# Optimization experiments

Measured on AMD Instinct MI355X. Metric: run time of the kernel, lower is better.

Reference implementation:

```python
import jax, jax.numpy as jnp
import numpy as np

B, T, S, I, H = 64, 64, 512, 512, 512

def setup_inputs() -> dict:
    key = jax.random.key(0)
    ks = jax.random.split(key, 9)
    sc = 0.02
    return {
        "input": jax.random.normal(ks[0], (B, T, I), jnp.float32),
        "h0": jax.random.normal(ks[1], (B, H), jnp.float32),
        "c0": jax.random.normal(ks[2], (B, H), jnp.float32),
        "ctx": jax.random.normal(ks[3], (S, B, H), jnp.float32),
        "W_ih": jax.random.normal(ks[4], (4 * H, I), jnp.float32) * sc,
        "b_ih": jax.random.normal(ks[5], (4 * H,), jnp.float32) * sc,
        "W_hh": jax.random.normal(ks[6], (4 * H, H), jnp.float32) * sc,
        "b_hh": jax.random.normal(ks[7], (4 * H,), jnp.float32) * sc,
        "W_out": jax.random.normal(ks[8], (H, 2 * H), jnp.float32) * sc,
    }

def reference(input, h0, c0, ctx, W_ih, b_ih, W_hh, b_hh, W_out):
    ctx_b = ctx.transpose(1, 0, 2)          # (B, S, H)
    x_tm = input.transpose(1, 0, 2)          # (T, B, I) time-major

    def step(carry, x):
        hx, cx = carry
        gates = x @ W_ih.T + b_ih + hx @ W_hh.T + b_hh   # (B, 4H)
        i, f, g, o = jnp.split(gates, 4, axis=1)          # chunk order: in, forget, cell, out
        ct = jax.nn.sigmoid(f) * cx + jax.nn.sigmoid(i) * jnp.tanh(g)
        ht = jax.nn.sigmoid(o) * jnp.tanh(ct)
        # dot attention over source positions
        scores = jnp.einsum('bsh,bh->bs', ctx_b, ht)      # (B, S)
        attn = jax.nn.softmax(scores, axis=1)
        wc = jnp.einsum('bs,bsh->bh', attn, ctx_b)        # (B, H)
        h_tilde = jnp.tanh(jnp.concatenate([wc, ht], axis=1) @ W_out.T)
        return (ht, ct), h_tilde

    (hT, cT), out = jax.lax.scan(step, (h0, c0), x_tm)    # out: (T, B, H)
    return out.transpose(1, 0, 2), hT, cT
```

## Files before the change

### kernel.cpp

```cpp
#include <hip/hip_runtime.h>
#include <hip/hip_bf16.h>

#define NB 64
#define NT_ 64
#define NS 512
#define NI 512
#define NH 512
#define G4 2048
#define H2 1024
#define BT (NB*NT_)
#define RBLK 64
#define CPB 8

typedef __attribute__((ext_vector_type(8))) short short8;
typedef __attribute__((ext_vector_type(4))) float f32x4;

__device__ __forceinline__ short f2bs(float f) {
    __hip_bfloat16 h = __float2bfloat16(f);
    return *reinterpret_cast<short*>(&h);
}
__device__ __forceinline__ float bs2f(short s) {
    unsigned int u = ((unsigned int)(unsigned short)s) << 16;
    union { unsigned int u; float f; } c; c.u = u; return c.f;
}
__device__ __forceinline__ short8 ld8b(const __hip_bfloat16* p) {
    return *reinterpret_cast<const short8*>(p);
}
__device__ __forceinline__ void ld8f2(const float* p, short8& hi, short8& lo) {
    float4 a = *reinterpret_cast<const float4*>(p);
    float4 b = *reinterpret_cast<const float4*>(p + 4);
    float v[8] = {a.x,a.y,a.z,a.w,b.x,b.y,b.z,b.w};
    #pragma unroll
    for (int i = 0; i < 8; i++) {
        short h = f2bs(v[i]);
        hi[i] = h;
        lo[i] = f2bs(v[i] - bs2f(h));
    }
}
__device__ __forceinline__ float fsigm(float x){ return 1.f/(1.f + __expf(-x)); }
__device__ __forceinline__ float ftanh(float x){ float e = __expf(2.f*x); return 1.f - 2.f/(e + 1.f); }

__global__ __launch_bounds__(256) void conv_split(const float* __restrict__ s,
                                                  __hip_bfloat16* __restrict__ hi,
                                                  __hip_bfloat16* __restrict__ lo, int n) {
    for (int i = blockIdx.x*256 + threadIdx.x; i < n; i += gridDim.x*256) {
        float x = s[i];
        __hip_bfloat16 h = __float2bfloat16(x);
        hi[i] = h;
        lo[i] = __float2bfloat16(x - __bfloat162float(h));
    }
}

__global__ __launch_bounds__(256) void hseq0_init(const float* __restrict__ h0,
                                                  __hip_bfloat16* __restrict__ hs_h,
                                                  __hip_bfloat16* __restrict__ hs_l,
                                                  unsigned* __restrict__ flags) {
    int i = blockIdx.x*256 + threadIdx.x;
    if (i < RBLK*32) flags[i] = 0u;
    if (i < NB*NH) {
        float x = h0[i];
        __hip_bfloat16 h = __float2bfloat16(x);
        hs_h[i] = h;
        hs_l[i] = __float2bfloat16(x - __bfloat162float(h));
    }
}

__global__ __launch_bounds__(256) void transpose_ctx(const float* __restrict__ ctx,
                                                     __hip_bfloat16* __restrict__ ctxT) {
    __shared__ float tile[64][65];
    int s0 = blockIdx.x*64, h0 = blockIdx.y*64, b = blockIdx.z;
    int tx = threadIdx.x & 63, ty = threadIdx.x >> 6;
    for (int i = 0; i < 16; i++) {
        int s = i*4 + ty;
        tile[s][tx] = ctx[(size_t)(s0+s)*NB*NH + (size_t)b*NH + h0 + tx];
    }
    __syncthreads();
    for (int i = 0; i < 16; i++) {
        int h = i*4 + ty;
        ctxT[(size_t)b*NH*NS + (size_t)(h0+h)*NS + s0 + tx] = __float2bfloat16(tile[tx][h]);
    }
}

__global__ __launch_bounds__(256) void gemm_xw(const __hip_bfloat16* __restrict__ Xh,
                                               const __hip_bfloat16* __restrict__ Xl,
                                               const __hip_bfloat16* __restrict__ Wh,
                                               const __hip_bfloat16* __restrict__ Wl,
                                               const float* __restrict__ b_ih,
                                               const float* __restrict__ b_hh,
                                               float* __restrict__ XW) {
    int wid = blockIdx.x*4 + (threadIdx.x>>6);
    int lane = threadIdx.x & 63;
    int m0 = (wid >> 5) * 64;
    int n0 = (wid & 31) * 64;
    int fr = lane & 15, fq = lane >> 4;
    f32x4 acc[4][4] = {};
    for (int kk = 0; kk < NI; kk += 32) {
        short8 ah[4], al[4], bh[4], bl[4];
        #pragma unroll
        for (int i = 0; i < 4; i++) {
            size_t off = (size_t)(m0+i*16+fr)*NI + kk + fq*8;
            ah[i] = ld8b(Xh + off);
            al[i] = ld8b(Xl + off);
        }
        #pragma unroll
        for (int j = 0; j < 4; j++) {
            bh[j] = ld8b(Wh + (size_t)(n0+j*16+fr)*NI + kk + fq*8);
            bl[j] = ld8b(Wl + (size_t)(n0+j*16+fr)*NI + kk + fq*8);
        }
        #pragma unroll
        for (int i = 0; i < 4; i++)
            #pragma unroll
            for (int j = 0; j < 4; j++) {
                acc[i][j] = __builtin_amdgcn_mfma_f32_16x16x32_bf16(ah[i], bh[j], acc[i][j], 0,0,0);
                acc[i][j] = __builtin_amdgcn_mfma_f32_16x16x32_bf16(ah[i], bl[j], acc[i][j], 0,0,0);
                acc[i][j] = __builtin_amdgcn_mfma_f32_16x16x32_bf16(al[i], bh[j], acc[i][j], 0,0,0);
            }
    }
    #pragma unroll
    for (int i = 0; i < 4; i++)
      #pragma unroll
      for (int j = 0; j < 4; j++)
        #pragma unroll
        for (int r = 0; r < 4; r++) {
            int m = m0 + i*16 + fq*4 + r;
            int n = n0 + j*16 + fr;
            XW[(size_t)m*G4 + n] = acc[i][j][r] + b_ih[n] + b_hh[n];
        }
}

__global__ __launch_bounds__(256, 1) void lstm_persist(
    const float* __restrict__ c0,
    const __hip_bfloat16* __restrict__ Whh_h,
    const __hip_bfloat16* __restrict__ Whh_l,
    const float* __restrict__ XW,
    __hip_bfloat16* __restrict__ hs_h,
    __hip_bfloat16* __restrict__ hs_l,
    float* __restrict__ hT, float* __restrict__ cT,
    unsigned* __restrict__ flags)
{
    __shared__ __hip_bfloat16 Wh[32*512];
    __shared__ __hip_bfloat16 Wl[32*512];
    __shared__ float gl[4][32][33];
    int tid = threadIdx.x, bi = blockIdx.x;
    int lane = tid & 63, w = tid >> 6;
    int fr = lane & 15, fq = lane >> 4;

    {
        int jl = tid >> 3, ck8 = tid & 7;
        int grow = (jl >> 3) * NH + bi * CPB + (jl & 7);
        const short8* srcH = (const short8*)(Whh_h + (size_t)grow * NH);
        const short8* srcL = (const short8*)(Whh_l + (size_t)grow * NH);
        #pragma unroll
        for (int cc = 0; cc < 8; cc++) {
            int ck = ck8 * 8 + cc;
            int sw = (ck * 16) ^ ((jl & 7) << 4);
            *(short8*)((char*)Wh + jl * 1024 + sw) = srcH[ck];
            *(short8*)((char*)Wl + jl * 1024 + sw) = srcL[ck];
        }
    }
    int eb  = tid >> 2;
    int ec0 = (tid & 3) * 2;
    int ebl = eb & 31, mhalf = eb >> 5;
    float creg[2];
    creg[0] = c0[eb * NH + bi*CPB + ec0];
    creg[1] = c0[eb * NH + bi*CPB + ec0 + 1];
    float xw[8];
    #pragma unroll
    for (int g = 0; g < 4; g++)
      #pragma unroll
      for (int u = 0; u < 2; u++)
        xw[g*2+u] = XW[(size_t)eb*NT_*G4 + g*NH + bi*CPB + ec0 + u];
    __syncthreads();

    int m0 = (w & 1) * 32;
    int kbase = (w >> 1) * 256;

    for (int t = 0; t < NT_; t++) {
        const __hip_bfloat16* Ah = hs_h + (size_t)t * NB * NH;
        const __hip_bfloat16* Al = hs_l + (size_t)t * NB * NH;

        short8 Aregh[2][8], Aregl[2][8];
        #pragma unroll
        for (int i = 0; i < 2; i++) {
            const __hip_bfloat16* rowH = Ah + (size_t)(m0 + i*16 + fr) * NH + kbase + fq*8;
            const __hip_bfloat16* rowL = Al + (size_t)(m0 + i*16 + fr) * NH + kbase + fq*8;
            #pragma unroll
            for (int k8 = 0; k8 < 8; k8++) {
                Aregh[i][k8] = ld8b(rowH + k8*32);
                Aregl[i][k8] = ld8b(rowL + k8*32);
            }
        }

        f32x4 acc[2][2] = {};
        #pragma unroll
        for (int k8 = 0; k8 < 8; k8++) {
            short8 b_h[2], b_l[2];
            #pragma unroll
            for (int j = 0; j < 2; j++) {
                int jl = j*16 + fr;
                int byt = jl*1024 + ((((kbase + k8*32 + fq*8)*2)) ^ ((jl & 7) << 4));
                b_h[j] = *(const short8*)((const char*)Wh + byt);
                b_l[j] = *(const short8*)((const char*)Wl + byt);
            }
            #pragma unroll
            for (int i = 0; i < 2; i++)
                #pragma unroll
                for (int j = 0; j < 2; j++) {
                    acc[i][j] = __builtin_amdgcn_mfma_f32_16x16x32_bf16(Aregh[i][k8], b_h[j], acc[i][j], 0,0,0);
                    acc[i][j] = __builtin_amdgcn_mfma_f32_16x16x32_bf16(Aregh[i][k8], b_l[j], acc[i][j], 0,0,0);
                    acc[i][j] = __builtin_amdgcn_mfma_f32_16x16x32_bf16(Aregl[i][k8], b_h[j], acc[i][j], 0,0,0);
                }
        }
        #pragma unroll
        for (int i = 0; i < 2; i++)
          #pragma unroll
          for (int j = 0; j < 2; j++)
            #pragma unroll
            for (int r = 0; r < 4; r++)
                gl[w][i*16 + fq*4 + r][j*16 + fr] = acc[i][j][r];
        __syncthreads();

        float hv[2];
        #pragma unroll
        for (int u = 0; u < 2; u++) {
            int cl = ec0 + u;
            float gi = gl[mhalf][ebl][cl]      + gl[2+mhalf][ebl][cl]      + xw[u];
            float gf = gl[mhalf][ebl][8 + cl]  + gl[2+mhalf][ebl][8 + cl]  + xw[2+u];
            float gg = gl[mhalf][ebl][16 + cl] + gl[2+mhalf][ebl][16 + cl] + xw[4+u];
            float go = gl[mhalf][ebl][24 + cl] + gl[2+mhalf][ebl][24 + cl] + xw[6+u];
            float ct = fsigm(gf)*creg[u] + fsigm(gi)*ftanh(gg);
            hv[u] = fsigm(go)*ftanh(ct);
            creg[u] = ct;
        }
        int hcol = bi*CPB + ec0;
        size_t hoff = (size_t)(t+1)*NB*NH + (size_t)eb*NH + hcol;
        unsigned short h0b = (unsigned short)f2bs(hv[0]);
        unsigned short h1b = (unsigned short)f2bs(hv[1]);
        unsigned ph = (unsigned)h0b | ((unsigned)h1b << 16);
        unsigned short l0b = (unsigned short)f2bs(hv[0] - bs2f((short)h0b));
        unsigned short l1b = (unsigned short)f2bs(hv[1] - bs2f((short)h1b));
        unsigned pl = (unsigned)l0b | ((unsigned)l1b << 16);
        __hip_atomic_store((unsigned*)&hs_h[hoff], ph, __ATOMIC_RELAXED, __HIP_MEMORY_SCOPE_AGENT);
        __hip_atomic_store((unsigned*)&hs_l[hoff], pl, __ATOMIC_RELAXED, __HIP_MEMORY_SCOPE_AGENT);
        if (t == NT_-1) {
            *(float2*)&hT[(size_t)eb*NH + hcol] = make_float2(hv[0], hv[1]);
            *(float2*)&cT[(size_t)eb*NH + hcol] = make_float2(creg[0], creg[1]);
        }

        asm volatile("s_waitcnt vmcnt(0)" ::: "memory");
        __syncthreads();
        if (tid == 0)
            __hip_atomic_store(&flags[bi*32], (unsigned)(t+1), __ATOMIC_RELAXED, __HIP_MEMORY_SCOPE_AGENT);
        if (t + 1 < NT_) {
            #pragma unroll
            for (int g = 0; g < 4; g++)
              #pragma unroll
              for (int u = 0; u < 2; u++)
                xw[g*2+u] = XW[((size_t)eb*NT_ + (t+1))*G4 + g*NH + bi*CPB + ec0 + u];
        }
        {
            unsigned target = (unsigned)(t+1);
            int guard = 0;
            while (__hip_atomic_load(&flags[lane*32], __ATOMIC_RELAXED, __HIP_MEMORY_SCOPE_AGENT) < target) {
                __builtin_amdgcn_s_sleep(1);
                if (++guard > (1<<22)) break;
            }
        }
    }
}

__global__ __launch_bounds__(256) void gemm_scores(const __hip_bfloat16* __restrict__ hs_h,
                                                   const __hip_bfloat16* __restrict__ hs_l,
                                                   const float* __restrict__ ctx,
                                                   float* __restrict__ scores) {
    int wid = blockIdx.x*4 + (threadIdx.x>>6);
    int lane = threadIdx.x & 63;
    int b  = wid >> 3;
    int n0 = (wid & 7) * 64;
    int fr = lane & 15, fq = lane >> 4;
    const __hip_bfloat16* Abh = hs_h + NB*NH + (size_t)b*NH;
    const __hip_bfloat16* Abl = hs_l + NB*NH + (size_t)b*NH;
    const float* Bb = ctx + (size_t)b*NH;
    f32x4 acc[4][4] = {};
    for (int kk = 0; kk < NH; kk += 32) {
        short8 ah[4], al[4], bh[4], bl[4];
        #pragma unroll
        for (int i = 0; i < 4; i++) {
            size_t off = (size_t)(i*16+fr)*NB*NH + kk + fq*8;
            ah[i] = ld8b(Abh + off);
            al[i] = ld8b(Abl + off);
        }
        #pragma unroll
        for (int j = 0; j < 4; j++) ld8f2(Bb + (size_t)(n0+j*16+fr)*NB*NH + kk + fq*8, bh[j], bl[j]);
        #pragma unroll
        for (int i = 0; i < 4; i++)
            #pragma unroll
            for (int j = 0; j < 4; j++) {
                acc[i][j] = __builtin_amdgcn_mfma_f32_16x16x32_bf16(ah[i], bh[j], acc[i][j], 0,0,0);
                acc[i][j] = __builtin_amdgcn_mfma_f32_16x16x32_bf16(ah[i], bl[j], acc[i][j], 0,0,0);
                acc[i][j] = __builtin_amdgcn_mfma_f32_16x16x32_bf16(al[i], bh[j], acc[i][j], 0,0,0);
            }
    }
    #pragma unroll
    for (int i = 0; i < 4; i++)
      #pragma unroll
      for (int j = 0; j < 4; j++)
        #pragma unroll
        for (int r = 0; r < 4; r++) {
            int t = i*16 + fq*4 + r;
            int s = n0 + j*16 + fr;
            scores[((size_t)b*NT_ + t)*NS + s] = acc[i][j][r];
        }
}

__global__ __launch_bounds__(256) void softmax_rows(const float* __restrict__ scores,
                                                    __hip_bfloat16* __restrict__ ah,
                                                    __hip_bfloat16* __restrict__ al) {
    int row = blockIdx.x*4 + (threadIdx.x>>6);
    int lane = threadIdx.x & 63;
    const float* r = scores + (size_t)row*NS;
    float v[8], mx = -1e30f;
    #pragma unroll
    for (int i = 0; i < 8; i++) { v[i] = r[lane + i*64]; mx = fmaxf(mx, v[i]); }
    #pragma unroll
    for (int off = 32; off; off >>= 1) mx = fmaxf(mx, __shfl_xor(mx, off));
    float sum = 0.f;
    #pragma unroll
    for (int i = 0; i < 8; i++) { v[i] = __expf(v[i]-mx); sum += v[i]; }
    #pragma unroll
    for (int off = 32; off; off >>= 1) sum += __shfl_xor(sum, off);
    float inv = 1.f/sum;
    #pragma unroll
    for (int i = 0; i < 8; i++) {
        float a = v[i]*inv;
        __hip_bfloat16 h = __float2bfloat16(a);
        ah[(size_t)row*NS + lane + i*64] = h;
        al[(size_t)row*NS + lane + i*64] = __float2bfloat16(a - __bfloat162float(h));
    }
}

__global__ __launch_bounds__(256) void gemm_wc(const __hip_bfloat16* __restrict__ Ah,
                                               const __hip_bfloat16* __restrict__ Al,
                                               const __hip_bfloat16* __restrict__ ctxT,
                                               float* __restrict__ Wc) {
    int wid = blockIdx.x*4 + (threadIdx.x>>6);
    int lane = threadIdx.x & 63;
    int b  = wid >> 3;
    int n0 = (wid & 7) * 64;
    int fr = lane & 15, fq = lane >> 4;
    const __hip_bfloat16* Abh = Ah + (size_t)b*NT_*NS;
    const __hip_bfloat16* Abl = Al + (size_t)b*NT_*NS;
    const __hip_bfloat16* Bb  = ctxT + (size_t)b*NH*NS;
    f32x4 acc[4][4] = {};
    for (int kk = 0; kk < NS; kk += 32) {
        short8 ah[4], al[4], bb[4];
        #pragma unroll
        for (int i = 0; i < 4; i++) {
            ah[i] = ld8b(Abh + (size_t)(i*16+fr)*NS + kk + fq*8);
            al[i] = ld8b(Abl + (size_t)(i*16+fr)*NS + kk + fq*8);
        }
        #pragma unroll
        for (int j = 0; j < 4; j++) bb[j] = ld8b(Bb + (size_t)(n0+j*16+fr)*NS + kk + fq*8);
        #pragma unroll
        for (int i = 0; i < 4; i++)
            #pragma unroll
            for (int j = 0; j < 4; j++) {
                acc[i][j] = __builtin_amdgcn_mfma_f32_16x16x32_bf16(ah[i], bb[j], acc[i][j], 0,0,0);
                acc[i][j] = __builtin_amdgcn_mfma_f32_16x16x32_bf16(al[i], bb[j], acc[i][j], 0,0,0);
            }
    }
    #pragma unroll
    for (int i = 0; i < 4; i++)
      #pragma unroll
      for (int j = 0; j < 4; j++)
        #pragma unroll
        for (int r = 0; r < 4; r++) {
            int t = i*16 + fq*4 + r;
            int h = n0 + j*16 + fr;
            Wc[((size_t)b*NT_ + t)*NH + h] = acc[i][j][r];
        }
}

__global__ __launch_bounds__(256) void gemm_out(const float* __restrict__ Wc,
                                                const __hip_bfloat16* __restrict__ hs_h,
                                                const __hip_bfloat16* __restrict__ hs_l,
                                                const __hip_bfloat16* __restrict__ Wh,
                                                const __hip_bfloat16* __restrict__ Wl,
                                                float* __restrict__ out) {
    int wid = blockIdx.x*4 + (threadIdx.x>>6);
    int lane = threadIdx.x & 63;
    int m0 = (wid >> 3) * 64;
    int n0 = (wid & 7) * 64;
    int fr = lane & 15, fq = lane >> 4;
    f32x4 acc[4][4] = {};
    for (int kk = 0; kk < NH; kk += 32) {
        short8 ah[4], al[4], bh[4], bl[4];
        #pragma unroll
        for (int i = 0; i < 4; i++) ld8f2(Wc + (size_t)(m0+i*16+fr)*NH + kk + fq*8, ah[i], al[i]);
        #pragma unroll
        for (int j = 0; j < 4; j++) {
            bh[j] = ld8b(Wh + (size_t)(n0+j*16+fr)*H2 + kk + fq*8);
            bl[j] = ld8b(Wl + (size_t)(n0+j*16+fr)*H2 + kk + fq*8);
        }
        #pragma unroll
        for (int i = 0; i < 4; i++)
            #pragma unroll
            for (int j = 0; j < 4; j++) {
                acc[i][j] = __builtin_amdgcn_mfma_f32_16x16x32_bf16(ah[i], bh[j], acc[i][j], 0,0,0);
                acc[i][j] = __builtin_amdgcn_mfma_f32_16x16x32_bf16(ah[i], bl[j], acc[i][j], 0,0,0);
                acc[i][j] = __builtin_amdgcn_mfma_f32_16x16x32_bf16(al[i], bh[j], acc[i][j], 0,0,0);
            }
    }
    {
        const __hip_bfloat16* A2h = hs_h + NB*NH + (size_t)(m0>>6)*NH;
        const __hip_bfloat16* A2l = hs_l + NB*NH + (size_t)(m0>>6)*NH;
        for (int kk = 0; kk < NH; kk += 32) {
            short8 ah[4], al[4], bh[4], bl[4];
            #pragma unroll
            for (int i = 0; i < 4; i++) {
                size_t off = (size_t)(i*16+fr)*NB*NH + kk + fq*8;
                ah[i] = ld8b(A2h + off);
                al[i] = ld8b(A2l + off);
            }
            #pragma unroll
            for (int j = 0; j < 4; j++) {
                bh[j] = ld8b(Wh + (size_t)(n0+j*16+fr)*H2 + NH + kk + fq*8);
                bl[j] = ld8b(Wl + (size_t)(n0+j*16+fr)*H2 + NH + kk + fq*8);
            }
            #pragma unroll
            for (int i = 0; i < 4; i++)
                #pragma unroll
                for (int j = 0; j < 4; j++) {
                    acc[i][j] = __builtin_amdgcn_mfma_f32_16x16x32_bf16(ah[i], bh[j], acc[i][j], 0,0,0);
                    acc[i][j] = __builtin_amdgcn_mfma_f32_16x16x32_bf16(ah[i], bl[j], acc[i][j], 0,0,0);
                    acc[i][j] = __builtin_amdgcn_mfma_f32_16x16x32_bf16(al[i], bh[j], acc[i][j], 0,0,0);
                }
        }
    }
    #pragma unroll
    for (int i = 0; i < 4; i++)
      #pragma unroll
      for (int j = 0; j < 4; j++)
        #pragma unroll
        for (int r = 0; r < 4; r++) {
            int m = m0 + i*16 + fq*4 + r;
            int n = n0 + j*16 + fr;
            out[(size_t)m*NH + n] = ftanh(acc[i][j][r]);
        }
}


extern "C" void kernel_launch(void* const* d_in, const int* in_sizes, int n_in,
                              void* d_out, int out_size, void* d_ws, size_t ws_size,
                              hipStream_t stream) {
    const float* input = (const float*)d_in[0];
    const float* h0    = (const float*)d_in[1];
    const float* c0    = (const float*)d_in[2];
    const float* ctx   = (const float*)d_in[3];
    const float* W_ih  = (const float*)d_in[4];
    const float* b_ih  = (const float*)d_in[5];
    const float* W_hh  = (const float*)d_in[6];
    const float* b_hh  = (const float*)d_in[7];
    const float* W_out = (const float*)d_in[8];
    float* out = (float*)d_out;

    const size_t OFF_XW     = 0;
    const size_t OFF_SCORES = 0;
    const size_t OFF_ATTN_H = 8388608;
    const size_t OFF_ATTN_L = 12582912;
    const size_t OFF_HS_H   = 33554432;
    const size_t OFF_HS_L   = 37814272;
    const size_t OFF_FLAGS  = 42074112;
    const size_t OFF_WC     = 42082304;
    const size_t OFF_XH     = 42082304;
    const size_t OFF_XL     = 46276608;
    const size_t OFF_WIH_H  = 50470912;
    const size_t OFF_WIH_L  = 52568064;
    const size_t OFF_WHH_H  = 54665216;
    const size_t OFF_WHH_L  = 56762368;
    const size_t OFF_WOUT_H = 58859520;
    const size_t OFF_WOUT_L = 59908096;
    const size_t OFF_CTXT   = 60956672;
    if (ws_size < 94511104u) return;

    char* ws = (char*)d_ws;
    float*          XW     = (float*)(ws + OFF_XW);
    float*          scores = (float*)(ws + OFF_SCORES);
    __hip_bfloat16* attn_h = (__hip_bfloat16*)(ws + OFF_ATTN_H);
    __hip_bfloat16* attn_l = (__hip_bfloat16*)(ws + OFF_ATTN_L);
    __hip_bfloat16* hs_h   = (__hip_bfloat16*)(ws + OFF_HS_H);
    __hip_bfloat16* hs_l   = (__hip_bfloat16*)(ws + OFF_HS_L);
    unsigned*       flags  = (unsigned*)(ws + OFF_FLAGS);
    float*          Wc     = (float*)(ws + OFF_WC);
    __hip_bfloat16* Xh     = (__hip_bfloat16*)(ws + OFF_XH);
    __hip_bfloat16* Xl     = (__hip_bfloat16*)(ws + OFF_XL);
    __hip_bfloat16* Wih_h  = (__hip_bfloat16*)(ws + OFF_WIH_H);
    __hip_bfloat16* Wih_l  = (__hip_bfloat16*)(ws + OFF_WIH_L);
    __hip_bfloat16* Whh_h  = (__hip_bfloat16*)(ws + OFF_WHH_H);
    __hip_bfloat16* Whh_l  = (__hip_bfloat16*)(ws + OFF_WHH_L);
    __hip_bfloat16* Wout_h = (__hip_bfloat16*)(ws + OFF_WOUT_H);
    __hip_bfloat16* Wout_l = (__hip_bfloat16*)(ws + OFF_WOUT_L);
    __hip_bfloat16* ctxT   = (__hip_bfloat16*)(ws + OFF_CTXT);

    conv_split<<<2048, 256, 0, stream>>>(W_ih, Wih_h, Wih_l, G4*NI);
    conv_split<<<2048, 256, 0, stream>>>(W_hh, Whh_h, Whh_l, G4*NH);
    conv_split<<<1024, 256, 0, stream>>>(W_out, Wout_h, Wout_l, NH*H2);
    conv_split<<<2048, 256, 0, stream>>>(input, Xh, Xl, BT*NI);
    hseq0_init<<<128, 256, 0, stream>>>(h0, hs_h, hs_l, flags);
    gemm_xw<<<512, 256, 0, stream>>>(Xh, Xl, Wih_h, Wih_l, b_ih, b_hh, XW);

    float* hT = out + (size_t)BT*NH;
    float* cT = hT + NB*NH;
    lstm_persist<<<RBLK, 256, 0, stream>>>(c0, Whh_h, Whh_l, XW, hs_h, hs_l, hT, cT, flags);

    transpose_ctx<<<dim3(8,8,64), 256, 0, stream>>>(ctx, ctxT);
    gemm_scores<<<128, 256, 0, stream>>>(hs_h, hs_l, ctx, scores);
    softmax_rows<<<1024, 256, 0, stream>>>(scores, attn_h, attn_l);
    gemm_wc<<<128, 256, 0, stream>>>(attn_h, attn_l, ctxT, Wc);
    gemm_out<<<128, 256, 0, stream>>>(Wc, hs_h, hs_l, Wout_h, Wout_l, out);
}
```

Before: 666.9 us.

## Replace flag-based grid barrier with sentinel-polled data-driven sync in persistent LSTM

Drops the per-step global flag barrier in the persistent LSTM kernel. Consumers now poll the hidden-state buffers directly, which are pre-filled with 0xFFFFFFFF sentinels, until valid data appears. The gate scratch is double-buffered so only one block barrier per step remains, and the XOR swizzle of the weight tile is replaced with row padding. The aim is to remove the full grid-wide flag round-trip and its extra barriers per timestep. The cost is filling a large sentinel region in the init kernel, and correctness now depends on bf16 pairs never legitimately equalling the sentinel pattern.

```diff
diff --git a/kernel.cpp b/kernel.cpp
--- a/kernel.cpp
+++ b/kernel.cpp
@@ -11,6 +11,7 @@
 #define BT (NB*NT_)
 #define RBLK 64
 #define CPB 8
+#define WROW 528
 
 typedef __attribute__((ext_vector_type(8))) short short8;
 typedef __attribute__((ext_vector_type(4))) float f32x4;
@@ -25,6 +26,14 @@
 }
 __device__ __forceinline__ short8 ld8b(const __hip_bfloat16* p) {
     return *reinterpret_cast<const short8*>(p);
+}
+__device__ __forceinline__ short8 mk8(unsigned long long a, unsigned long long b) {
+    union { unsigned long long q[2]; short8 s; } u;
+    u.q[0] = a; u.q[1] = b;
+    return u.s;
+}
+__device__ __forceinline__ bool okq(unsigned long long q) {
+    return ((unsigned)q != 0xFFFFFFFFu) && ((unsigned)(q >> 32) != 0xFFFFFFFFu);
 }
 __device__ __forceinline__ void ld8f2(const float* p, short8& hi, short8& lo) {
     float4 a = *reinterpret_cast<const float4*>(p);
@@ -53,15 +62,25 @@
 
 __global__ __launch_bounds__(256) void hseq0_init(const float* __restrict__ h0,
                                                   __hip_bfloat16* __restrict__ hs_h,
-                                                  __hip_bfloat16* __restrict__ hs_l,
-                                                  unsigned* __restrict__ flags) {
+                                                  __hip_bfloat16* __restrict__ hs_l) {
     int i = blockIdx.x*256 + threadIdx.x;
-    if (i < RBLK*32) flags[i] = 0u;
-    if (i < NB*NH) {
-        float x = h0[i];
-        __hip_bfloat16 h = __float2bfloat16(x);
-        hs_h[i] = h;
-        hs_l[i] = __float2bfloat16(x - __bfloat162float(h));
+    const int nsent = NB*NH*NT_/2;
+    unsigned* ph = (unsigned*)(hs_h + NB*NH);
+    unsigned* pl = (unsigned*)(hs_l + NB*NH);
+    for (int k = i; k < nsent; k += gridDim.x*256) {
+        __hip_atomic_store(&ph[k], 0xFFFFFFFFu, __ATOMIC_RELAXED, __HIP_MEMORY_SCOPE_AGENT);
+        __hip_atomic_store(&pl[k], 0xFFFFFFFFu, __ATOMIC_RELAXED, __HIP_MEMORY_SCOPE_AGENT);
+    }
+    if (i < NB*NH/2) {
+        float v0 = h0[2*i], v1 = h0[2*i+1];
+        unsigned short h0b = (unsigned short)f2bs(v0);
+        unsigned short h1b = (unsigned short)f2bs(v1);
+        unsigned short l0b = (unsigned short)f2bs(v0 - bs2f((short)h0b));
+        unsigned short l1b = (unsigned short)f2bs(v1 - bs2f((short)h1b));
+        __hip_atomic_store((unsigned*)hs_h + i, (unsigned)h0b | ((unsigned)h1b << 16),
+                           __ATOMIC_RELAXED, __HIP_MEMORY_SCOPE_AGENT);
+        __hip_atomic_store((unsigned*)hs_l + i, (unsigned)l0b | ((unsigned)l1b << 16),
+                           __ATOMIC_RELAXED, __HIP_MEMORY_SCOPE_AGENT);
     }
 }
 
@@ -135,12 +154,11 @@
     const float* __restrict__ XW,
     __hip_bfloat16* __restrict__ hs_h,
     __hip_bfloat16* __restrict__ hs_l,
-    float* __restrict__ hT, float* __restrict__ cT,
-    unsigned* __restrict__ flags)
+    float* __restrict__ hT, float* __restrict__ cT)
 {
-    __shared__ __hip_bfloat16 Wh[32*512];
-    __shared__ __hip_bfloat16 Wl[32*512];
-    __shared__ float gl[4][32][33];
+    __shared__ __hip_bfloat16 Wh[32*WROW];
+    __shared__ __hip_bfloat16 Wl[32*WROW];
+    __shared__ float gl[2][4][32][33];
     int tid = threadIdx.x, bi = blockIdx.x;
     int lane = tid & 63, w = tid >> 6;
     int fr = lane & 15, fq = lane >> 4;
@@ -153,9 +171,8 @@
         #pragma unroll
         for (int cc = 0; cc < 8; cc++) {
             int ck = ck8 * 8 + cc;
-            int sw = (ck * 16) ^ ((jl & 7) << 4);
-            *(short8*)((char*)Wh + jl * 1024 + sw) = srcH[ck];
-            *(short8*)((char*)Wl + jl * 1024 + sw) = srcL[ck];
+            *(short8*)((char*)Wh + jl*(WROW*2) + ck*16) = srcH[ck];
+            *(short8*)((char*)Wl + jl*(WROW*2) + ck*16) = srcL[ck];
         }
     }
     int eb  = tid >> 2;
@@ -176,19 +193,39 @@
     int kbase = (w >> 1) * 256;
 
     for (int t = 0; t < NT_; t++) {
-        const __hip_bfloat16* Ah = hs_h + (size_t)t * NB * NH;
-        const __hip_bfloat16* Al = hs_l + (size_t)t * NB * NH;
-
-        short8 Aregh[2][8], Aregl[2][8];
-        #pragma unroll
-        for (int i = 0; i < 2; i++) {
-            const __hip_bfloat16* rowH = Ah + (size_t)(m0 + i*16 + fr) * NH + kbase + fq*8;
-            const __hip_bfloat16* rowL = Al + (size_t)(m0 + i*16 + fr) * NH + kbase + fq*8;
-            #pragma unroll
-            for (int k8 = 0; k8 < 8; k8++) {
-                Aregh[i][k8] = ld8b(rowH + k8*32);
-                Aregl[i][k8] = ld8b(rowL + k8*32);
-            }
+        int p = t & 1;
+
+        unsigned long long qa[2][8][2], ql[2][8][2];
+        {
+            const char* bH0 = (const char*)(hs_h + (size_t)t*NB*NH + (size_t)(m0+fr)*NH + kbase);
+            const char* bL0 = (const char*)(hs_l + (size_t)t*NB*NH + (size_t)(m0+fr)*NH + kbase);
+            const char* bH1 = bH0 + 16*NH*2;
+            const char* bL1 = bL0 + 16*NH*2;
+            int guard = 0; bool ok;
+            do {
+                ok = true;
+                #pragma unroll
+                for (int i = 0; i < 2; i++) {
+                    const char* bH = i ? bH1 : bH0;
+                    const char* bL = i ? bL1 : bL0;
+                    #pragma unroll
+                    for (int k8 = 0; k8 < 8; k8++) {
+                        unsigned long long* pH = (unsigned long long*)(bH + k8*64 + fq*16);
+                        unsigned long long* pL = (unsigned long long*)(bL + k8*64 + fq*16);
+                        qa[i][k8][0] = __hip_atomic_load(pH,   __ATOMIC_RELAXED, __HIP_MEMORY_SCOPE_AGENT);
+                        qa[i][k8][1] = __hip_atomic_load(pH+1, __ATOMIC_RELAXED, __HIP_MEMORY_SCOPE_AGENT);
+                        ql[i][k8][0] = __hip_atomic_load(pL,   __ATOMIC_RELAXED, __HIP_MEMORY_SCOPE_AGENT);
+                        ql[i][k8][1] = __hip_atomic_load(pL+1, __ATOMIC_RELAXED, __HIP_MEMORY_SCOPE_AGENT);
+                    }
+                }
+                #pragma unroll
+                for (int i = 0; i < 2; i++)
+                  #pragma unroll
+                  for (int k8 = 0; k8 < 8; k8++)
+                    ok = ok && okq(qa[i][k8][0]) && okq(qa[i][k8][1])
+                            && okq(ql[i][k8][0]) && okq(ql[i][k8][1]);
+                if (!__all(ok)) __builtin_amdgcn_s_sleep(1);
+            } while (!__all(ok) && ++guard < (1<<22));
         }
 
         f32x4 acc[2][2] = {};
@@ -198,18 +235,21 @@
             #pragma unroll
             for (int j = 0; j < 2; j++) {
                 int jl = j*16 + fr;
-                int byt = jl*1024 + ((((kbase + k8*32 + fq*8)*2)) ^ ((jl & 7) << 4));
+                int byt = jl*(WROW*2) + (kbase + k8*32 + fq*8)*2;
                 b_h[j] = *(const short8*)((const char*)Wh + byt);
                 b_l[j] = *(const short8*)((const char*)Wl + byt);
             }
             #pragma unroll
-            for (int i = 0; i < 2; i++)
+            for (int i = 0; i < 2; i++) {
+                short8 a_h = mk8(qa[i][k8][0], qa[i][k8][1]);
+                short8 a_l = mk8(ql[i][k8][0], ql[i][k8][1]);
                 #pragma unroll
                 for (int j = 0; j < 2; j++) {
-                    acc[i][j] = __builtin_amdgcn_mfma_f32_16x16x32_bf16(Aregh[i][k8], b_h[j], acc[i][j], 0,0,0);
-                    acc[i][j] = __builtin_amdgcn_mfma_f32_16x16x32_bf16(Aregh[i][k8], b_l[j], acc[i][j], 0,0,0);
-                    acc[i][j] = __builtin_amdgcn_mfma_f32_16x16x32_bf16(Aregl[i][k8], b_h[j], acc[i][j], 0,0,0);
+                    acc[i][j] = __builtin_amdgcn_mfma_f32_16x16x32_bf16(a_h, b_h[j], acc[i][j], 0,0,0);
+                    acc[i][j] = __builtin_amdgcn_mfma_f32_16x16x32_bf16(a_h, b_l[j], acc[i][j], 0,0,0);
+                    acc[i][j] = __builtin_amdgcn_mfma_f32_16x16x32_bf16(a_l, b_h[j], acc[i][j], 0,0,0);
                 }
+            }
         }
         #pragma unroll
         for (int i = 0; i < 2; i++)
@@ -217,17 +257,21 @@
           for (int j = 0; j < 2; j++)
             #pragma unroll
             for (int r = 0; r < 4; r++)
-                gl[w][i*16 + fq*4 + r][j*16 + fr] = acc[i][j][r];
-        __syncthreads();
+                gl[p][w][i*16 + fq*4 + r][j*16 + fr] = acc[i][j][r];
+
+        __builtin_amdgcn_sched_barrier(0);
+        asm volatile("s_waitcnt lgkmcnt(0)" ::: "memory");
+        __builtin_amdgcn_s_barrier();
+        __builtin_amdgcn_sched_barrier(0);
 
         float hv[2];
         #pragma unroll
         for (int u = 0; u < 2; u++) {
             int cl = ec0 + u;
-            float gi = gl[mhalf][ebl][cl]      + gl[2+mhalf][ebl][cl]      + xw[u];
-            float gf = gl[mhalf][ebl][8 + cl]  + gl[2+mhalf][ebl][8 + cl]  + xw[2+u];
-            float gg = gl[mhalf][ebl][16 + cl] + gl[2+mhalf][ebl][16 + cl] + xw[4+u];
-            float go = gl[mhalf][ebl][24 + cl] + gl[2+mhalf][ebl][24 + cl] + xw[6+u];
+            float gi = gl[p][mhalf][ebl][cl]      + gl[p][2+mhalf][ebl][cl]      + xw[u];
+            float gf = gl[p][mhalf][ebl][8 + cl]  + gl[p][2+mhalf][ebl][8 + cl]  + xw[2+u];
+            float gg = gl[p][mhalf][ebl][16 + cl] + gl[p][2+mhalf][ebl][16 + cl] + xw[4+u];
+            float go = gl[p][mhalf][ebl][24 + cl] + gl[p][2+mhalf][ebl][24 + cl] + xw[6+u];
             float ct = fsigm(gf)*creg[u] + fsigm(gi)*ftanh(gg);
             hv[u] = fsigm(go)*ftanh(ct);
             creg[u] = ct;
@@ -246,25 +290,12 @@
             *(float2*)&hT[(size_t)eb*NH + hcol] = make_float2(hv[0], hv[1]);
             *(float2*)&cT[(size_t)eb*NH + hcol] = make_float2(creg[0], creg[1]);
         }
-
-        asm volatile("s_waitcnt vmcnt(0)" ::: "memory");
-        __syncthreads();
-        if (tid == 0)
-            __hip_atomic_store(&flags[bi*32], (unsigned)(t+1), __ATOMIC_RELAXED, __HIP_MEMORY_SCOPE_AGENT);
         if (t + 1 < NT_) {
             #pragma unroll
             for (int g = 0; g < 4; g++)
               #pragma unroll
               for (int u = 0; u < 2; u++)
                 xw[g*2+u] = XW[((size_t)eb*NT_ + (t+1))*G4 + g*NH + bi*CPB + ec0 + u];
-        }
-        {
-            unsigned target = (unsigned)(t+1);
-            int guard = 0;
-            while (__hip_atomic_load(&flags[lane*32], __ATOMIC_RELAXED, __HIP_MEMORY_SCOPE_AGENT) < target) {
-                __builtin_amdgcn_s_sleep(1);
-                if (++guard > (1<<22)) break;
-            }
         }
     }
 }
@@ -470,7 +501,6 @@
     const size_t OFF_ATTN_L = 12582912;
     const size_t OFF_HS_H   = 33554432;
     const size_t OFF_HS_L   = 37814272;
-    const size_t OFF_FLAGS  = 42074112;
     const size_t OFF_WC     = 42082304;
     const size_t OFF_XH     = 42082304;
     const size_t OFF_XL     = 46276608;
@@ -490,7 +520,6 @@
     __hip_bfloat16* attn_l = (__hip_bfloat16*)(ws + OFF_ATTN_L);
     __hip_bfloat16* hs_h   = (__hip_bfloat16*)(ws + OFF_HS_H);
     __hip_bfloat16* hs_l   = (__hip_bfloat16*)(ws + OFF_HS_L);
-    unsigned*       flags  = (unsigned*)(ws + OFF_FLAGS);
     float*          Wc     = (float*)(ws + OFF_WC);
     __hip_bfloat16* Xh     = (__hip_bfloat16*)(ws + OFF_XH);
     __hip_bfloat16* Xl     = (__hip_bfloat16*)(ws + OFF_XL);
@@ -506,12 +535,12 @@
     conv_split<<<2048, 256, 0, stream>>>(W_hh, Whh_h, Whh_l, G4*NH);
     conv_split<<<1024, 256, 0, stream>>>(W_out, Wout_h, Wout_l, NH*H2);
     conv_split<<<2048, 256, 0, stream>>>(input, Xh, Xl, BT*NI);
-    hseq0_init<<<128, 256, 0, stream>>>(h0, hs_h, hs_l, flags);
+    hseq0_init<<<128, 256, 0, stream>>>(h0, hs_h, hs_l);
     gemm_xw<<<512, 256, 0, stream>>>(Xh, Xl, Wih_h, Wih_l, b_ih, b_hh, XW);
 
     float* hT = out + (size_t)BT*NH;
     float* cT = hT + NB*NH;
-    lstm_persist<<<RBLK, 256, 0, stream>>>(c0, Whh_h, Whh_l, XW, hs_h, hs_l, hT, cT, flags);
+    lstm_persist<<<RBLK, 256, 0, stream>>>(c0, Whh_h, Whh_l, XW, hs_h, hs_l, hT, cT);
 
     transpose_ctx<<<dim3(8,8,64), 256, 0, stream>>>(ctx, ctxT);
     gemm_scores<<<128, 256, 0, stream>>>(hs_h, hs_l, ctx, scores);
```

Measured after the change: 1.074 ms. 61.0% more time.

## Merge input GEMM, ctx transpose and W_out split into persistent LSTM megakernel

Applied to the files above, without the earlier changes.

Folds the input-projection GEMM, the ctx transpose and the W_out bf16 split into one launch alongside the persistent LSTM recurrence, using block-ID ranges to pick the role. The XW GEMM is re-tiled to produce one timestep per block group, and it signals per-timestep counters that the recurrent blocks spin on. This lets the serial recurrence start before the whole input GEMM finishes and overlaps the independent prep work with it. The risks are that the spin-wait ordering depends on the recurrent blocks being scheduled first, and the large grid with 82KB shared memory per block lowers occupancy for the helper roles.

```diff
diff --git a/kernel.cpp b/kernel.cpp
--- a/kernel.cpp
+++ b/kernel.cpp
@@ -11,6 +11,10 @@
 #define BT (NB*NT_)
 #define RBLK 64
 #define CPB 8
+#define XWB 512
+#define TRB 4096
+#define WOB 128
+#define GRID_MEGA (RBLK + XWB + TRB + WOB)
 
 typedef __attribute__((ext_vector_type(8))) short short8;
 typedef __attribute__((ext_vector_type(4))) float f32x4;
@@ -54,9 +58,9 @@
 __global__ __launch_bounds__(256) void hseq0_init(const float* __restrict__ h0,
                                                   __hip_bfloat16* __restrict__ hs_h,
                                                   __hip_bfloat16* __restrict__ hs_l,
-                                                  unsigned* __restrict__ flags) {
+                                                  unsigned* __restrict__ sync) {
     int i = blockIdx.x*256 + threadIdx.x;
-    if (i < RBLK*32) flags[i] = 0u;
+    if (i < 2048) sync[i] = 0u;
     if (i < NB*NH) {
         float x = h0[i];
         __hip_bfloat16 h = __float2bfloat16(x);
@@ -65,206 +69,239 @@
     }
 }
 
-__global__ __launch_bounds__(256) void transpose_ctx(const float* __restrict__ ctx,
-                                                     __hip_bfloat16* __restrict__ ctxT) {
-    __shared__ float tile[64][65];
-    int s0 = blockIdx.x*64, h0 = blockIdx.y*64, b = blockIdx.z;
-    int tx = threadIdx.x & 63, ty = threadIdx.x >> 6;
-    for (int i = 0; i < 16; i++) {
-        int s = i*4 + ty;
-        tile[s][tx] = ctx[(size_t)(s0+s)*NB*NH + (size_t)b*NH + h0 + tx];
-    }
-    __syncthreads();
-    for (int i = 0; i < 16; i++) {
-        int h = i*4 + ty;
-        ctxT[(size_t)b*NH*NS + (size_t)(h0+h)*NS + s0 + tx] = __float2bfloat16(tile[tx][h]);
-    }
-}
-
-__global__ __launch_bounds__(256) void gemm_xw(const __hip_bfloat16* __restrict__ Xh,
-                                               const __hip_bfloat16* __restrict__ Xl,
-                                               const __hip_bfloat16* __restrict__ Wh,
-                                               const __hip_bfloat16* __restrict__ Wl,
-                                               const float* __restrict__ b_ih,
-                                               const float* __restrict__ b_hh,
-                                               float* __restrict__ XW) {
-    int wid = blockIdx.x*4 + (threadIdx.x>>6);
-    int lane = threadIdx.x & 63;
-    int m0 = (wid >> 5) * 64;
-    int n0 = (wid & 31) * 64;
-    int fr = lane & 15, fq = lane >> 4;
-    f32x4 acc[4][4] = {};
-    for (int kk = 0; kk < NI; kk += 32) {
-        short8 ah[4], al[4], bh[4], bl[4];
-        #pragma unroll
-        for (int i = 0; i < 4; i++) {
-            size_t off = (size_t)(m0+i*16+fr)*NI + kk + fq*8;
-            ah[i] = ld8b(Xh + off);
-            al[i] = ld8b(Xl + off);
-        }
-        #pragma unroll
-        for (int j = 0; j < 4; j++) {
-            bh[j] = ld8b(Wh + (size_t)(n0+j*16+fr)*NI + kk + fq*8);
-            bl[j] = ld8b(Wl + (size_t)(n0+j*16+fr)*NI + kk + fq*8);
-        }
-        #pragma unroll
-        for (int i = 0; i < 4; i++)
-            #pragma unroll
-            for (int j = 0; j < 4; j++) {
-                acc[i][j] = __builtin_amdgcn_mfma_f32_16x16x32_bf16(ah[i], bh[j], acc[i][j], 0,0,0);
-                acc[i][j] = __builtin_amdgcn_mfma_f32_16x16x32_bf16(ah[i], bl[j], acc[i][j], 0,0,0);
-                acc[i][j] = __builtin_amdgcn_mfma_f32_16x16x32_bf16(al[i], bh[j], acc[i][j], 0,0,0);
-            }
-    }
-    #pragma unroll
-    for (int i = 0; i < 4; i++)
-      #pragma unroll
-      for (int j = 0; j < 4; j++)
-        #pragma unroll
-        for (int r = 0; r < 4; r++) {
-            int m = m0 + i*16 + fq*4 + r;
-            int n = n0 + j*16 + fr;
-            XW[(size_t)m*G4 + n] = acc[i][j][r] + b_ih[n] + b_hh[n];
-        }
-}
-
-__global__ __launch_bounds__(256, 1) void lstm_persist(
+__global__ __launch_bounds__(256, 1) void lstm_mega(
     const float* __restrict__ c0,
     const __hip_bfloat16* __restrict__ Whh_h,
     const __hip_bfloat16* __restrict__ Whh_l,
-    const float* __restrict__ XW,
+    const __hip_bfloat16* __restrict__ Xh,
+    const __hip_bfloat16* __restrict__ Xl,
+    const __hip_bfloat16* __restrict__ Wih_h,
+    const __hip_bfloat16* __restrict__ Wih_l,
+    const float* __restrict__ b_ih,
+    const float* __restrict__ b_hh,
+    float* __restrict__ XW2,
     __hip_bfloat16* __restrict__ hs_h,
     __hip_bfloat16* __restrict__ hs_l,
     float* __restrict__ hT, float* __restrict__ cT,
-    unsigned* __restrict__ flags)
+    unsigned* __restrict__ flags,
+    unsigned* __restrict__ xwcnt,
+    const float* __restrict__ ctx,
+    __hip_bfloat16* __restrict__ ctxT,
+    const float* __restrict__ W_out,
+    __hip_bfloat16* __restrict__ Wout_h,
+    __hip_bfloat16* __restrict__ Wout_l)
 {
-    __shared__ __hip_bfloat16 Wh[32*512];
-    __shared__ __hip_bfloat16 Wl[32*512];
-    __shared__ float gl[4][32][33];
-    int tid = threadIdx.x, bi = blockIdx.x;
+    __shared__ __align__(16) char smem_raw[82432];
+    int bid = blockIdx.x;
+    int tid = threadIdx.x;
     int lane = tid & 63, w = tid >> 6;
     int fr = lane & 15, fq = lane >> 4;
 
-    {
-        int jl = tid >> 3, ck8 = tid & 7;
-        int grow = (jl >> 3) * NH + bi * CPB + (jl & 7);
-        const short8* srcH = (const short8*)(Whh_h + (size_t)grow * NH);
-        const short8* srcL = (const short8*)(Whh_l + (size_t)grow * NH);
-        #pragma unroll
-        for (int cc = 0; cc < 8; cc++) {
-            int ck = ck8 * 8 + cc;
-            int sw = (ck * 16) ^ ((jl & 7) << 4);
-            *(short8*)((char*)Wh + jl * 1024 + sw) = srcH[ck];
-            *(short8*)((char*)Wl + jl * 1024 + sw) = srcL[ck];
-        }
-    }
-    int eb  = tid >> 2;
-    int ec0 = (tid & 3) * 2;
-    int ebl = eb & 31, mhalf = eb >> 5;
-    float creg[2];
-    creg[0] = c0[eb * NH + bi*CPB + ec0];
-    creg[1] = c0[eb * NH + bi*CPB + ec0 + 1];
-    float xw[8];
-    #pragma unroll
-    for (int g = 0; g < 4; g++)
-      #pragma unroll
-      for (int u = 0; u < 2; u++)
-        xw[g*2+u] = XW[(size_t)eb*NT_*G4 + g*NH + bi*CPB + ec0 + u];
-    __syncthreads();
-
-    int m0 = (w & 1) * 32;
-    int kbase = (w >> 1) * 256;
-
-    for (int t = 0; t < NT_; t++) {
-        const __hip_bfloat16* Ah = hs_h + (size_t)t * NB * NH;
-        const __hip_bfloat16* Al = hs_l + (size_t)t * NB * NH;
-
-        short8 Aregh[2][8], Aregl[2][8];
-        #pragma unroll
-        for (int i = 0; i < 2; i++) {
-            const __hip_bfloat16* rowH = Ah + (size_t)(m0 + i*16 + fr) * NH + kbase + fq*8;
-            const __hip_bfloat16* rowL = Al + (size_t)(m0 + i*16 + fr) * NH + kbase + fq*8;
+    if (bid < RBLK) {
+        __hip_bfloat16* Wh = (__hip_bfloat16*)smem_raw;
+        __hip_bfloat16* Wl = (__hip_bfloat16*)(smem_raw + 32768);
+        float (*gl)[32][33] = (float(*)[32][33])(smem_raw + 65536);
+        int bi = bid;
+
+        {
+            int jl = tid >> 3, ck8 = tid & 7;
+            int grow = (jl >> 3) * NH + bi * CPB + (jl & 7);
+            const short8* srcH = (const short8*)(Whh_h + (size_t)grow * NH);
+            const short8* srcL = (const short8*)(Whh_l + (size_t)grow * NH);
+            #pragma unroll
+            for (int cc = 0; cc < 8; cc++) {
+                int ck = ck8 * 8 + cc;
+                int sw = (ck * 16) ^ ((jl & 7) << 4);
+                *(short8*)((char*)Wh + jl * 1024 + sw) = srcH[ck];
+                *(short8*)((char*)Wl + jl * 1024 + sw) = srcL[ck];
+            }
+        }
+        int eb  = tid >> 2;
+        int ec0 = (tid & 3) * 2;
+        int ebl = eb & 31, mhalf = eb >> 5;
+        float creg[2];
+        creg[0] = c0[eb * NH + bi*CPB + ec0];
+        creg[1] = c0[eb * NH + bi*CPB + ec0 + 1];
+        {
+            int guard = 0;
+            while (__hip_atomic_load(&xwcnt[0], __ATOMIC_RELAXED, __HIP_MEMORY_SCOPE_AGENT) < 8u) {
+                __builtin_amdgcn_s_sleep(1);
+                if (++guard > (1<<22)) break;
+            }
+        }
+        float xw[8];
+        #pragma unroll
+        for (int g = 0; g < 4; g++)
+          #pragma unroll
+          for (int u = 0; u < 2; u++)
+            xw[g*2+u] = XW2[(size_t)eb*G4 + g*NH + bi*CPB + ec0 + u];
+        __syncthreads();
+
+        int m0 = (w & 1) * 32;
+        int kbase = (w >> 1) * 256;
+
+        for (int t = 0; t < NT_; t++) {
+            const __hip_bfloat16* Ah = hs_h + (size_t)t * NB * NH;
+            const __hip_bfloat16* Al = hs_l + (size_t)t * NB * NH;
+
+            short8 Aregh[2][8], Aregl[2][8];
+            #pragma unroll
+            for (int i = 0; i < 2; i++) {
+                const __hip_bfloat16* rowH = Ah + (size_t)(m0 + i*16 + fr) * NH + kbase + fq*8;
+                const __hip_bfloat16* rowL = Al + (size_t)(m0 + i*16 + fr) * NH + kbase + fq*8;
+                #pragma unroll
+                for (int k8 = 0; k8 < 8; k8++) {
+                    Aregh[i][k8] = ld8b(rowH + k8*32);
+                    Aregl[i][k8] = ld8b(rowL + k8*32);
+                }
+            }
+
+            f32x4 acc[2][2] = {};
             #pragma unroll
             for (int k8 = 0; k8 < 8; k8++) {
-                Aregh[i][k8] = ld8b(rowH + k8*32);
-                Aregl[i][k8] = ld8b(rowL + k8*32);
-            }
-        }
-
-        f32x4 acc[2][2] = {};
-        #pragma unroll
-        for (int k8 = 0; k8 < 8; k8++) {
-            short8 b_h[2], b_l[2];
-            #pragma unroll
-            for (int j = 0; j < 2; j++) {
-                int jl = j*16 + fr;
-                int byt = jl*1024 + ((((kbase + k8*32 + fq*8)*2)) ^ ((jl & 7) << 4));
-                b_h[j] = *(const short8*)((const char*)Wh + byt);
-                b_l[j] = *(const short8*)((const char*)Wl + byt);
+                short8 b_h[2], b_l[2];
+                #pragma unroll
+                for (int j = 0; j < 2; j++) {
+                    int jl = j*16 + fr;
+                    int byt = jl*1024 + ((((kbase + k8*32 + fq*8)*2)) ^ ((jl & 7) << 4));
+                    b_h[j] = *(const short8*)((const char*)Wh + byt);
+                    b_l[j] = *(const short8*)((const char*)Wl + byt);
+                }
+                #pragma unroll
+                for (int i = 0; i < 2; i++)
+                    #pragma unroll
+                    for (int j = 0; j < 2; j++) {
+                        acc[i][j] = __builtin_amdgcn_mfma_f32_16x16x32_bf16(Aregh[i][k8], b_h[j], acc[i][j], 0,0,0);
+                        acc[i][j] = __builtin_amdgcn_mfma_f32_16x16x32_bf16(Aregh[i][k8], b_l[j], acc[i][j], 0,0,0);
+                        acc[i][j] = __builtin_amdgcn_mfma_f32_16x16x32_bf16(Aregl[i][k8], b_h[j], acc[i][j], 0,0,0);
+                    }
             }
             #pragma unroll
             for (int i = 0; i < 2; i++)
-                #pragma unroll
-                for (int j = 0; j < 2; j++) {
-                    acc[i][j] = __builtin_amdgcn_mfma_f32_16x16x32_bf16(Aregh[i][k8], b_h[j], acc[i][j], 0,0,0);
-                    acc[i][j] = __builtin_amdgcn_mfma_f32_16x16x32_bf16(Aregh[i][k8], b_l[j], acc[i][j], 0,0,0);
-                    acc[i][j] = __builtin_amdgcn_mfma_f32_16x16x32_bf16(Aregl[i][k8], b_h[j], acc[i][j], 0,0,0);
+              #pragma unroll
+              for (int j = 0; j < 2; j++)
+                #pragma unroll
+                for (int r = 0; r < 4; r++)
+                    gl[w][i*16 + fq*4 + r][j*16 + fr] = acc[i][j][r];
+            __syncthreads();
+
+            float hv[2];
+            #pragma unroll
+            for (int u = 0; u < 2; u++) {
+                int cl = ec0 + u;
+                float gi = gl[mhalf][ebl][cl]      + gl[2+mhalf][ebl][cl]      + xw[u];
+                float gf = gl[mhalf][ebl][8 + cl]  + gl[2+mhalf][ebl][8 + cl]  + xw[2+u];
+                float gg = gl[mhalf][ebl][16 + cl] + gl[2+mhalf][ebl][16 + cl] + xw[4+u];
+                float go = gl[mhalf][ebl][24 + cl] + gl[2+mhalf][ebl][24 + cl] + xw[6+u];
+                float ct = fsigm(gf)*creg[u] + fsigm(gi)*ftanh(gg);
+                hv[u] = fsigm(go)*ftanh(ct);
+                creg[u] = ct;
+            }
+            int hcol = bi*CPB + ec0;
+            size_t hoff = (size_t)(t+1)*NB*NH + (size_t)eb*NH + hcol;
+            unsigned short h0b = (unsigned short)f2bs(hv[0]);
+            unsigned short h1b = (unsigned short)f2bs(hv[1]);
+            unsigned ph = (unsigned)h0b | ((unsigned)h1b << 16);
+            unsigned short l0b = (unsigned short)f2bs(hv[0] - bs2f((short)h0b));
+            unsigned short l1b = (unsigned short)f2bs(hv[1] - bs2f((short)h1b));
+            unsigned pl = (unsigned)l0b | ((unsigned)l1b << 16);
+            __hip_atomic_store((unsigned*)&hs_h[hoff], ph, __ATOMIC_RELAXED, __HIP_MEMORY_SCOPE_AGENT);
+            __hip_atomic_store((unsigned*)&hs_l[hoff], pl, __ATOMIC_RELAXED, __HIP_MEMORY_SCOPE_AGENT);
+            if (t == NT_-1) {
+                *(float2*)&hT[(size_t)eb*NH + hcol] = make_float2(hv[0], hv[1]);
+                *(float2*)&cT[(size_t)eb*NH + hcol] = make_float2(creg[0], creg[1]);
+            }
+
+            asm volatile("s_waitcnt vmcnt(0)" ::: "memory");
+            __syncthreads();
+            if (tid == 0)
+                __hip_atomic_store(&flags[bi*16], (unsigned)(t+1), __ATOMIC_RELAXED, __HIP_MEMORY_SCOPE_AGENT);
+            if (t + 1 < NT_) {
+                int guard = 0;
+                while (__hip_atomic_load(&xwcnt[(t+1)*16], __ATOMIC_RELAXED, __HIP_MEMORY_SCOPE_AGENT) < 8u) {
+                    __builtin_amdgcn_s_sleep(1);
+                    if (++guard > (1<<22)) break;
                 }
-        }
-        #pragma unroll
-        for (int i = 0; i < 2; i++)
+                #pragma unroll
+                for (int g = 0; g < 4; g++)
+                  #pragma unroll
+                  for (int u = 0; u < 2; u++)
+                    xw[g*2+u] = XW2[((size_t)(t+1)*NB + eb)*G4 + g*NH + bi*CPB + ec0 + u];
+            }
+            {
+                unsigned target = (unsigned)(t+1);
+                int guard = 0;
+                while (__hip_atomic_load(&flags[lane*16], __ATOMIC_RELAXED, __HIP_MEMORY_SCOPE_AGENT) < target) {
+                    __builtin_amdgcn_s_sleep(1);
+                    if (++guard > (1<<22)) break;
+                }
+            }
+        }
+    } else if (bid < RBLK + XWB) {
+        int e  = bid - RBLK;
+        int t0 = e >> 3;
+        int n0 = ((e & 7) * 4 + w) * 64;
+        f32x4 acc[4][4] = {};
+        for (int kk = 0; kk < NI; kk += 32) {
+            short8 ah[4], al[4], bh[4], bl[4];
+            #pragma unroll
+            for (int i = 0; i < 4; i++) {
+                size_t off = ((size_t)(i*16+fr)*NT_ + t0)*NI + kk + fq*8;
+                ah[i] = ld8b(Xh + off);
+                al[i] = ld8b(Xl + off);
+            }
+            #pragma unroll
+            for (int j = 0; j < 4; j++) {
+                bh[j] = ld8b(Wih_h + (size_t)(n0+j*16+fr)*NI + kk + fq*8);
+                bl[j] = ld8b(Wih_l + (size_t)(n0+j*16+fr)*NI + kk + fq*8);
+            }
+            #pragma unroll
+            for (int i = 0; i < 4; i++)
+                #pragma unroll
+                for (int j = 0; j < 4; j++) {
+                    acc[i][j] = __builtin_amdgcn_mfma_f32_16x16x32_bf16(ah[i], bh[j], acc[i][j], 0,0,0);
+                    acc[i][j] = __builtin_amdgcn_mfma_f32_16x16x32_bf16(ah[i], bl[j], acc[i][j], 0,0,0);
+                    acc[i][j] = __builtin_amdgcn_mfma_f32_16x16x32_bf16(al[i], bh[j], acc[i][j], 0,0,0);
+                }
+        }
+        #pragma unroll
+        for (int i = 0; i < 4; i++)
           #pragma unroll
-          for (int j = 0; j < 2; j++)
-            #pragma unroll
-            for (int r = 0; r < 4; r++)
-                gl[w][i*16 + fq*4 + r][j*16 + fr] = acc[i][j][r];
-        __syncthreads();
-
-        float hv[2];
-        #pragma unroll
-        for (int u = 0; u < 2; u++) {
-            int cl = ec0 + u;
-            float gi = gl[mhalf][ebl][cl]      + gl[2+mhalf][ebl][cl]      + xw[u];
-            float gf = gl[mhalf][ebl][8 + cl]  + gl[2+mhalf][ebl][8 + cl]  + xw[2+u];
-            float gg = gl[mhalf][ebl][16 + cl] + gl[2+mhalf][ebl][16 + cl] + xw[4+u];
-            float go = gl[mhalf][ebl][24 + cl] + gl[2+mhalf][ebl][24 + cl] + xw[6+u];
-            float ct = fsigm(gf)*creg[u] + fsigm(gi)*ftanh(gg);
-            hv[u] = fsigm(go)*ftanh(ct);
-            creg[u] = ct;
-        }
-        int hcol = bi*CPB + ec0;
-        size_t hoff = (size_t)(t+1)*NB*NH + (size_t)eb*NH + hcol;
-        unsigned short h0b = (unsigned short)f2bs(hv[0]);
-        unsigned short h1b = (unsigned short)f2bs(hv[1]);
-        unsigned ph = (unsigned)h0b | ((unsigned)h1b << 16);
-        unsigned short l0b = (unsigned short)f2bs(hv[0] - bs2f((short)h0b));
-        unsigned short l1b = (unsigned short)f2bs(hv[1] - bs2f((short)h1b));
-        unsigned pl = (unsigned)l0b | ((unsigned)l1b << 16);
-        __hip_atomic_store((unsigned*)&hs_h[hoff], ph, __ATOMIC_RELAXED, __HIP_MEMORY_SCOPE_AGENT);
-        __hip_atomic_store((unsigned*)&hs_l[hoff], pl, __ATOMIC_RELAXED, __HIP_MEMORY_SCOPE_AGENT);
-        if (t == NT_-1) {
-            *(float2*)&hT[(size_t)eb*NH + hcol] = make_float2(hv[0], hv[1]);
-            *(float2*)&cT[(size_t)eb*NH + hcol] = make_float2(creg[0], creg[1]);
-        }
-
+          for (int j = 0; j < 4; j++)
+            #pragma unroll
+            for (int r = 0; r < 4; r++) {
+                int b = i*16 + fq*4 + r;
+                int n = n0 + j*16 + fr;
+                float v = acc[i][j][r] + b_ih[n] + b_hh[n];
+                union { float f; unsigned u; } cv; cv.f = v;
+                __hip_atomic_store((unsigned*)&XW2[((size_t)t0*NB + b)*G4 + n], cv.u,
+                                   __ATOMIC_RELAXED, __HIP_MEMORY_SCOPE_AGENT);
+            }
         asm volatile("s_waitcnt vmcnt(0)" ::: "memory");
         __syncthreads();
         if (tid == 0)
-            __hip_atomic_store(&flags[bi*32], (unsigned)(t+1), __ATOMIC_RELAXED, __HIP_MEMORY_SCOPE_AGENT);
-        if (t + 1 < NT_) {
-            #pragma unroll
-            for (int g = 0; g < 4; g++)
-              #pragma unroll
-              for (int u = 0; u < 2; u++)
-                xw[g*2+u] = XW[((size_t)eb*NT_ + (t+1))*G4 + g*NH + bi*CPB + ec0 + u];
-        }
-        {
-            unsigned target = (unsigned)(t+1);
-            int guard = 0;
-            while (__hip_atomic_load(&flags[lane*32], __ATOMIC_RELAXED, __HIP_MEMORY_SCOPE_AGENT) < target) {
-                __builtin_amdgcn_s_sleep(1);
-                if (++guard > (1<<22)) break;
-            }
+            __hip_atomic_fetch_add(&xwcnt[t0*16], 1u, __ATOMIC_RELAXED, __HIP_MEMORY_SCOPE_AGENT);
+    } else if (bid < RBLK + XWB + TRB) {
+        float (*tile)[65] = (float(*)[65])smem_raw;
+        int tr = bid - (RBLK + XWB);
+        int s0 = (tr & 7) * 64, h0 = ((tr >> 3) & 7) * 64, b = tr >> 6;
+        int tx = tid & 63, ty = tid >> 6;
+        for (int i = 0; i < 16; i++) {
+            int s = i*4 + ty;
+            tile[s][tx] = ctx[(size_t)(s0+s)*NB*NH + (size_t)b*NH + h0 + tx];
+        }
+        __syncthreads();
+        for (int i = 0; i < 16; i++) {
+            int h = i*4 + ty;
+            ctxT[(size_t)b*NH*NS + (size_t)(h0+h)*NS + s0 + tx] = __float2bfloat16(tile[tx][h]);
+        }
+    } else {
+        int wv = bid - (RBLK + XWB + TRB);
+        for (int i = wv*256 + tid; i < NH*H2; i += WOB*256) {
+            float x = W_out[i];
+            __hip_bfloat16 h = __float2bfloat16(x);
+            Wout_h[i] = h;
+            Wout_l[i] = __float2bfloat16(x - __bfloat162float(h));
         }
     }
 }
@@ -470,7 +507,7 @@
     const size_t OFF_ATTN_L = 12582912;
     const size_t OFF_HS_H   = 33554432;
     const size_t OFF_HS_L   = 37814272;
-    const size_t OFF_FLAGS  = 42074112;
+    const size_t OFF_SYNC   = 42074112;
     const size_t OFF_WC     = 42082304;
     const size_t OFF_XH     = 42082304;
     const size_t OFF_XL     = 46276608;
@@ -484,13 +521,15 @@
     if (ws_size < 94511104u) return;
 
     char* ws = (char*)d_ws;
-    float*          XW     = (float*)(ws + OFF_XW);
+    float*          XW2    = (float*)(ws + OFF_XW);
     float*          scores = (float*)(ws + OFF_SCORES);
     __hip_bfloat16* attn_h = (__hip_bfloat16*)(ws + OFF_ATTN_H);
     __hip_bfloat16* attn_l = (__hip_bfloat16*)(ws + OFF_ATTN_L);
     __hip_bfloat16* hs_h   = (__hip_bfloat16*)(ws + OFF_HS_H);
     __hip_bfloat16* hs_l   = (__hip_bfloat16*)(ws + OFF_HS_L);
-    unsigned*       flags  = (unsigned*)(ws + OFF_FLAGS);
+    unsigned*       sync   = (unsigned*)(ws + OFF_SYNC);
+    unsigned*       flags  = sync;
+    unsigned*       xwcnt  = sync + 1024;
     float*          Wc     = (float*)(ws + OFF_WC);
     __hip_bfloat16* Xh     = (__hip_bfloat16*)(ws + OFF_XH);
     __hip_bfloat16* Xl     = (__hip_bfloat16*)(ws + OFF_XL);
@@ -504,16 +543,15 @@
 
     conv_split<<<2048, 256, 0, stream>>>(W_ih, Wih_h, Wih_l, G4*NI);
     conv_split<<<2048, 256, 0, stream>>>(W_hh, Whh_h, Whh_l, G4*NH);
-    conv_split<<<1024, 256, 0, stream>>>(W_out, Wout_h, Wout_l, NH*H2);
     conv_split<<<2048, 256, 0, stream>>>(input, Xh, Xl, BT*NI);
-    hseq0_init<<<128, 256, 0, stream>>>(h0, hs_h, hs_l, flags);
-    gemm_xw<<<512, 256, 0, stream>>>(Xh, Xl, Wih_h, Wih_l, b_ih, b_hh, XW);
+    hseq0_init<<<128, 256, 0, stream>>>(h0, hs_h, hs_l, sync);
 
     float* hT = out + (size_t)BT*NH;
     float* cT = hT + NB*NH;
-    lstm_persist<<<RBLK, 256, 0, stream>>>(c0, Whh_h, Whh_l, XW, hs_h, hs_l, hT, cT, flags);
-
-    transpose_ctx<<<dim3(8,8,64), 256, 0, stream>>>(ctx, ctxT);
+    lstm_mega<<<GRID_MEGA, 256, 0, stream>>>(c0, Whh_h, Whh_l, Xh, Xl, Wih_h, Wih_l,
+                                             b_ih, b_hh, XW2, hs_h, hs_l, hT, cT,
+                                             flags, xwcnt, ctx, ctxT, W_out, Wout_h, Wout_l);
+
     gemm_scores<<<128, 256, 0, stream>>>(hs_h, hs_l, ctx, scores);
     softmax_rows<<<1024, 256, 0, stream>>>(scores, attn_h, attn_l);
     gemm_wc<<<128, 256, 0, stream>>>(attn_h, attn_l, ctxT, Wc);
```

Result: faster. 635.6 us (-4.7%).
